# Optimization experiments

Measured on AMD Instinct MI355X. Metric: run time of the kernel, lower is better.

## Reference

```python
import jax, jax.numpy as jnp
from jax import lax
import numpy as np
import math

B, N, M, SIG, HID, NFEAT, OUT, H = 256, 512, 16, 256, 256, 3, 10, 256
ALPHA, BETA = 1.0, 0.5


def setup_inputs() -> dict:
    key = jax.random.key(0)
    ks = jax.random.split(key, 12)
    s_g = 1.0 / math.sqrt(HID)
    s_f = 1.0 / math.sqrt(SIG)
    return {
        "x": jax.random.normal(ks[0], (B, 1, H, H), jnp.float32),
        "unif": jax.random.uniform(ks[1], (B, N), jnp.float32),
        "z": jax.random.normal(ks[2], (B, N, 2), jnp.float32),
        "m_g_params": jax.random.normal(ks[3], (1, 6 * M), jnp.float32),
        "gc1_w": jax.random.uniform(ks[4], (NFEAT, HID), jnp.float32, -s_g, s_g),
        "gc1_b": jax.random.uniform(ks[5], (HID,), jnp.float32, -s_g, s_g),
        "gc2_w": jax.random.uniform(ks[6], (HID, HID), jnp.float32, -s_g, s_g),
        "gc2_b": jax.random.uniform(ks[7], (HID,), jnp.float32, -s_g, s_g),
        "collapser1": 0.1 * jax.random.normal(ks[8], (SIG, N), jnp.float32),
        "collapser2": 0.1 * jax.random.normal(ks[9], (SIG, N), jnp.float32),
        "fcf_w": jax.random.uniform(ks[10], (OUT, SIG), jnp.float32, -s_f, s_f),
        "fcf_b": jax.random.uniform(ks[11], (OUT,), jnp.float32, -s_f, s_f),
    }


def _mixture_fields(m_g_params):
    # torch: split [num_sample, 6M] into M chunks of 6, stack -> [M, N, 6],
    # split along last dim, then .view(N, M) in C-order on the [M, N] field.
    raw = m_g_params.reshape(M, 6)  # [M, 6]
    return [jnp.broadcast_to(raw[:, j][:, None], (M, N)).reshape(N, M) for j in range(6)]


def reference(x, unif, z, m_g_params, gc1_w, gc1_b, gc2_w, gc2_b,
              collapser1, collapser2, fcf_w, fcf_b):
    pi_f, mux_f, muy_f, sx_f, sy_f, rho_f = _mixture_fields(m_g_params)
    pi = jax.nn.softmax(pi_f, axis=-1)            # [N, M]
    # categorical sampling via CDF inversion, vectorized over batch
    cdf = jnp.cumsum(pi, axis=-1)                 # [N, M]
    idx = jnp.argmax(unif[:, :, None] < cdf[None], axis=-1)  # [B, N]
    row = jnp.arange(N)[None, :]
    gat = lambda f: f[row, idx]                   # [B, N]
    mux, muy = gat(mux_f), gat(muy_f)
    sx, sy = jnp.exp(gat(sx_f)), jnp.exp(gat(sy_f))
    rho = jnp.tanh(gat(rho_f))
    # reparameterized bivariate-normal sample via Cholesky (lower)
    z1, z2 = z[..., 0], z[..., 1]
    xs = mux + sx * z1
    ys = muy + sy * (rho * z1 + jnp.sqrt(1.0 - rho * rho) * z2)
    # torch MVN.sample() is no_grad -> detach samples
    xs_c, ys_c = lax.stop_gradient(xs), lax.stop_gradient(ys)
    dx, dy = xs_c - mux, ys_c - muy
    omr2 = 1.0 - rho * rho
    quad = (dx * dx / (sx * sx) - 2.0 * rho * dx * dy / (sx * sy) + dy * dy / (sy * sy)) / omr2
    logprob = (-jnp.log(2.0 * jnp.pi) - jnp.log(sx * sy)
               - 0.5 * jnp.log(omr2) - 0.5 * quad)  # [B, N]
    full_log_prob = logprob.sum(axis=-1)           # [B]
    loc = jnp.tanh(jnp.stack([xs_c, ys_c], axis=-1))  # [B, N, 2]
    # adjacency: inverse shifted pairwise squared distance
    diff = loc[:, :, None, :] - loc[:, None, :, :]  # [B, N, N, 2]
    adj = 1.0 / (ALPHA + BETA * jnp.sum(diff * diff, axis=-1))  # [B, N, N]
    # pixel gather: denormalize (trunc toward zero, like torch .long())
    pix = jnp.trunc(0.5 * (loc + 1.0) * H - 0.1).astype(jnp.int32)
    pix = jnp.clip(pix, 0, H - 1)
    bidx = jnp.arange(B)[:, None]
    pv = x[bidx, :, pix[..., 0], pix[..., 1]]      # [B, N, 1]
    feat = jnp.concatenate([pv, loc], axis=-1)     # [B, N, 3]
    # GCN (eval mode: no dropout)
    s1 = jax.nn.relu(jnp.einsum('bnm,bmh->bnh', adj, feat @ gc1_w) + gc1_b)
    s2 = jax.nn.relu(jnp.einsum('bnm,bmh->bnh', adj, s1 @ gc2_w) + gc2_b)
    # nn.Softmax() (no dim) on 3D input resolves to dim=0 in torch
    g1 = jax.nn.softmax(jnp.einsum('sn,bnh->bsh', collapser1, s1), axis=0)
    g2 = jax.nn.softmax(jnp.einsum('sn,bnh->bsh', collapser2, s2), axis=0)
    sig = (g1 + g2).sum(axis=2)                    # [B, SIG]
    out = jax.nn.softmax(sig @ fcf_w.T + fcf_b, axis=-1)  # [B, OUT]
    return out, full_log_prob
```

## Files before the change

kernel.cpp:

```cpp
#include <hip/hip_runtime.h>
#include <hip/hip_bf16.h>
#include <math.h>

#define Bx   256
#define Nx   512
#define SIGx 256
#define HIDx 256
#define OUTx 10
#define Hx   256

typedef __attribute__((ext_vector_type(4))) float f32x4;
typedef __attribute__((ext_vector_type(2))) uint uint2v;
typedef long fp8x8;
typedef unsigned char uchar;

#define WAITVM(N) asm volatile("s_waitcnt vmcnt(" #N ")" ::: "memory")
#define MEMFENCE() asm volatile("" ::: "memory")

__device__ inline uchar f2fp8(float v) {
    int r = __builtin_amdgcn_cvt_pk_fp8_f32(v, 0.0f, 0, false);
    return (uchar)(r & 0xff);
}
__device__ inline uint pk4fp8(float a0, float a1, float a2, float a3) {
    int r = __builtin_amdgcn_cvt_pk_fp8_f32(a0, a1, 0, false);
    r = __builtin_amdgcn_cvt_pk_fp8_f32(a2, a3, r, true);
    return (uint)r;
}

__device__ inline void gload_lds16(const uchar* g, uchar* l) {
    __builtin_amdgcn_global_load_lds(
        (const __attribute__((address_space(1))) uint*)g,
        (__attribute__((address_space(3))) uint*)l, 16, 0, 0);
}
__device__ inline const uchar* laddr(const uchar* base, int row, int kb) {
    int ps = (kb >> 4) ^ ((row >> 1) & 3) ^ ((row >> 4) & 3);
    return base + row*64 + ps*16 + (kb & 15);
}
__device__ inline const uchar* laddrB(const uchar* base, int row, int kb) {
    int ps = ((kb >> 4) & 7) ^ (row & 7);
    return base + row*128 + ps*16 + (kb & 15);
}

__global__ __launch_bounds__(512) void kA_sample(
    const float* __restrict__ x, const float* __restrict__ z,
    const float* __restrict__ mg, float* __restrict__ feat,
    float* __restrict__ flp)
{
    int b = blockIdx.x;
    int n = threadIdx.x;
    int g = n >> 5;
    float mux = mg[g*6+1];
    float muy = mg[g*6+2];
    float sxv = expf(mg[g*6+3]);
    float syv = expf(mg[g*6+4]);
    float rho = tanhf(mg[g*6+5]);
    float z1 = z[((size_t)b*Nx + n)*2 + 0];
    float z2 = z[((size_t)b*Nx + n)*2 + 1];
    float omr2 = 1.0f - rho*rho;
    float xs = mux + sxv*z1;
    float ys = muy + syv*(rho*z1 + sqrtf(omr2)*z2);
    float dx = xs - mux, dy = ys - muy;
    float quad = (dx*dx/(sxv*sxv) - 2.0f*rho*dx*dy/(sxv*syv) + dy*dy/(syv*syv)) / omr2;
    float logprob = -1.8378770664093453f - logf(sxv*syv) - 0.5f*logf(omr2) - 0.5f*quad;
    float lx = tanhf(xs), ly = tanhf(ys);
    int px = (int)truncf(0.5f*(lx+1.0f)*(float)Hx - 0.1f);
    int py = (int)truncf(0.5f*(ly+1.0f)*(float)Hx - 0.1f);
    px = px < 0 ? 0 : (px > Hx-1 ? Hx-1 : px);
    py = py < 0 ? 0 : (py > Hx-1 ? Hx-1 : py);
    float pv = x[(size_t)b*Hx*Hx + (size_t)px*Hx + py];
    size_t fo = ((size_t)b*Nx + n)*3;
    feat[fo+0] = pv; feat[fo+1] = lx; feat[fo+2] = ly;

    __shared__ float red[512];
    red[n] = logprob;
    __syncthreads();
    for (int st = 256; st > 0; st >>= 1) {
        if (n < st) red[n] += red[n+st];
        __syncthreads();
    }
    if (n == 0) flp[b] = red[0];
}

__global__ __launch_bounds__(256) void kPrep(
    const float* __restrict__ c1, const float* __restrict__ c2,
    const float* __restrict__ w2,
    uchar* __restrict__ c1q, uchar* __restrict__ c2q, uchar* __restrict__ w2tq)
{
    int idx = blockIdx.x*256 + threadIdx.x;
    if (idx < SIGx*Nx) {
        c1q[idx] = f2fp8(16.0f * c1[idx]);
        c2q[idx] = f2fp8(16.0f * c2[idx]);
    }
    if (idx < HIDx*HIDx) {
        int i = idx >> 8, j = idx & 255;
        w2tq[idx] = f2fp8(16.0f * w2[j*HIDx + i]);
    }
}

__global__ __launch_bounds__(512) void kFuse1S(
    const float* __restrict__ featL, const float* __restrict__ w1,
    const float* __restrict__ b1,
    uchar* __restrict__ adjAll, uchar* __restrict__ s1tAll)
{
    int b = blockIdx.x;
    int n0 = blockIdx.y * 256;
    const float* fb = featL + (size_t)b*Nx*3;
    uchar* adj = adjAll + (size_t)b*Nx*Nx;
    uchar* s1t = s1tAll + (size_t)b*HIDx*Nx;

    __shared__ float fpv[Nx], flx[Nx], fly[Nx], fH[Nx];
    __shared__ float w1s[3*HIDx], b1s[HIDx];
    __shared__ float Gp[8][3][256];

    int t = threadIdx.x;
    {
        float pv = fb[t*3+0], lx = fb[t*3+1], ly = fb[t*3+2];
        fpv[t] = pv; flx[t] = lx; fly[t] = ly;
        fH[t] = fmaf(0.5f*lx, lx, fmaf(0.5f*ly, ly, 1.0f));
    }
    for (int i = t; i < 3*HIDx; i += 512) w1s[i] = w1[i];
    if (t < HIDx) b1s[t] = b1[t];
    __syncthreads();

    int tq = t & 63;
    int mc = t >> 6;
    int lc = tq*4;
    int n4 = n0 + lc;

    float xn[4], yn[4], cn[4];
    #pragma unroll
    for (int e = 0; e < 4; ++e) {
        xn[e] = flx[n4+e]; yn[e] = fly[n4+e];
        cn[e] = fmaf(0.5f*xn[e], xn[e], 0.5f*yn[e]*yn[e]);
    }
    float G0[4] = {}, G1[4] = {}, G2[4] = {};

    int m0 = mc*64;
    #pragma unroll 4
    for (int mm = 0; mm < 64; ++mm) {
        int m = m0 + mm;
        float hx = fH[m], fx = flx[m], fy = fly[m];
        float a[4];
        #pragma unroll
        for (int e = 0; e < 4; ++e) {
            float s = fmaf(-yn[e], fy, fmaf(-xn[e], fx, hx + cn[e]));
            a[e] = __builtin_amdgcn_rcpf(s);
            G0[e] = fmaf(a[e], fpv[m], G0[e]);
            G1[e] = fmaf(a[e], fx, G1[e]);
            G2[e] = fmaf(a[e], fy, G2[e]);
        }
        *(uint*)(adj + (size_t)m*Nx + n4) = pk4fp8(a[0], a[1], a[2], a[3]);
    }

    *(f32x4*)&Gp[mc][0][lc] = (f32x4){G0[0],G0[1],G0[2],G0[3]};
    *(f32x4*)&Gp[mc][1][lc] = (f32x4){G1[0],G1[1],G1[2],G1[3]};
    *(f32x4*)&Gp[mc][2][lc] = (f32x4){G2[0],G2[1],G2[2],G2[3]};
    __syncthreads();

    f32x4 T0 = {}, T1 = {}, T2 = {};
    #pragma unroll
    for (int j = 0; j < 8; ++j) {
        T0 += *(const f32x4*)&Gp[j][0][lc];
        T1 += *(const f32x4*)&Gp[j][1][lc];
        T2 += *(const f32x4*)&Gp[j][2][lc];
    }

    int hc = mc;
    #pragma unroll 4
    for (int hh = 0; hh < 32; ++hh) {
        int h = hc*32 + hh;
        float w0 = w1s[h], wA = w1s[HIDx+h], wB = w1s[2*HIDx+h], bb = b1s[h];
        float v0 = fminf(fmaxf(fmaf(T0.x,w0, fmaf(T1.x,wA, fmaf(T2.x,wB, bb))), 0.0f), 448.0f);
        float v1 = fminf(fmaxf(fmaf(T0.y,w0, fmaf(T1.y,wA, fmaf(T2.y,wB, bb))), 0.0f), 448.0f);
        float v2 = fminf(fmaxf(fmaf(T0.z,w0, fmaf(T1.z,wA, fmaf(T2.z,wB, bb))), 0.0f), 448.0f);
        float v3 = fminf(fmaxf(fmaf(T0.w,w0, fmaf(T1.w,wA, fmaf(T2.w,wB, bb))), 0.0f), 448.0f);
        *(uint*)(s1t + (size_t)h*Nx + n4) = pk4fp8(v0, v1, v2, v3);
    }
}

__global__ __launch_bounds__(512, 4) void kGemmAdjB(
    const uchar* __restrict__ Aall, const uchar* __restrict__ adjAll,
    const float* __restrict__ bias, uchar* __restrict__ outAll)
{
    int b    = blockIdx.x;
    int tile = blockIdx.y;
    int rt = tile >> 2;
    int ct = tile & 3;
    const uchar* A = Aall + (size_t)b*HIDx*Nx;
    const uchar* Badj = adjAll + (size_t)b*Nx*Nx;
    uchar* outp = outAll + (size_t)b*HIDx*Nx;

    __shared__ __align__(16) uchar Als[2][128*128];
    __shared__ __align__(16) uchar Bls[2][128*128];
    int t = threadIdx.x;
    int lane = t & 63, wave = t >> 6;
    int wr = wave >> 2, wc = wave & 3;
    int q = lane >> 4, c16 = lane & 15;
    int r0 = rt*128, n0 = ct*128;
    int srow0 = t >> 3;
    int su0   = t & 7;
    f32x4 acc[4][2] = {};

    auto stage = [&](int buf, int kkv) {
        #pragma unroll
        for (int p = 0; p < 2; ++p) {
            int row = p*64 + srow0;
            int su = su0 ^ (row & 7);
            gload_lds16(A + (size_t)(r0+row)*Nx + kkv + su*16,
                        Als[buf] + p*8192 + wave*1024);
            gload_lds16(Badj + (size_t)(n0+row)*Nx + kkv + su*16,
                        Bls[buf] + p*8192 + wave*1024);
        }
    };

    const int nt = Nx/128;
    stage(0, 0);
    for (int i = 0; i < nt; ++i) {
        if (i < nt-1) { stage((i+1)&1, (i+1)*128); WAITVM(4); }
        else WAITVM(0);
        __builtin_amdgcn_s_barrier();
        MEMFENCE();
        const uchar* Ac = Als[i&1];
        const uchar* Bc = Bls[i&1];
        #pragma unroll
        for (int ks = 0; ks < 128; ks += 32) {
            fp8x8 af[4], bfr[2];
            #pragma unroll
            for (int i2 = 0; i2 < 4; ++i2)
                af[i2] = *(const fp8x8*)laddrB(Ac, wr*64 + i2*16 + c16, ks + q*8);
            #pragma unroll
            for (int j = 0; j < 2; ++j)
                bfr[j] = *(const fp8x8*)laddrB(Bc, wc*32 + j*16 + c16, ks + q*8);
            #pragma unroll
            for (int i2 = 0; i2 < 4; ++i2)
                #pragma unroll
                for (int j = 0; j < 2; ++j)
                    acc[i2][j] = __builtin_amdgcn_mfma_f32_16x16x32_fp8_fp8(af[i2], bfr[j], acc[i2][j], 0, 0, 0);
        }
        MEMFENCE();
        __builtin_amdgcn_s_barrier();
        MEMFENCE();
    }
    #pragma unroll
    for (int i = 0; i < 4; ++i) {
        int rowb = r0 + wr*64 + i*16 + q*4;
        #pragma unroll
        for (int j = 0; j < 2; ++j) {
            int col = n0 + wc*32 + j*16 + c16;
            #pragma unroll
            for (int r = 0; r < 4; ++r) {
                float v = fmaxf(acc[i][j][r] + bias[rowb + r], 0.0f) * 0.25f;
                outp[(size_t)(rowb + r)*Nx + col] = f2fp8(fminf(v, 448.0f));
            }
        }
    }
}

__global__ __launch_bounds__(512, 4) void kGstd8B(
    const uchar* __restrict__ Ash, const uchar* __restrict__ Ball,
    uchar* __restrict__ outAll, float oscale)
{
    int b    = blockIdx.x;
    int tile = blockIdx.y;
    int rt = tile >> 1;
    int ct = tile & 1;
    const uchar* B = Ball + (size_t)b*HIDx*Nx;
    uchar* outp = outAll + (size_t)b*HIDx*256;

    __shared__ __align__(16) uchar Als[2][128*128];
    __shared__ __align__(16) uchar Bls[2][128*128];
    int t = threadIdx.x;
    int lane = t & 63, wave = t >> 6;
    int wr = wave >> 2, wc = wave & 3;
    int q = lane >> 4, c16 = lane & 15;
    int r0 = rt*128, n0 = ct*128;
    int srow0 = t >> 3;
    int su0   = t & 7;
    f32x4 acc[4][2] = {};

    auto stage = [&](int buf, int kkv) {
        #pragma unroll
        for (int p = 0; p < 2; ++p) {
            int row = p*64 + srow0;
            int su = su0 ^ (row & 7);
            gload_lds16(Ash + (size_t)(r0+row)*Nx + kkv + su*16,
                        Als[buf] + p*8192 + wave*1024);
            gload_lds16(B + (size_t)(n0+row)*Nx + kkv + su*16,
                        Bls[buf] + p*8192 + wave*1024);
        }
    };

    const int nt = Nx/128;
    stage(0, 0);
    for (int i = 0; i < nt; ++i) {
        if (i < nt-1) { stage((i+1)&1, (i+1)*128); WAITVM(4); }
        else WAITVM(0);
        __builtin_amdgcn_s_barrier();
        MEMFENCE();
        const uchar* Ac = Als[i&1];
        const uchar* Bc = Bls[i&1];
        #pragma unroll
        for (int ks = 0; ks < 128; ks += 32) {
            fp8x8 af[4], bfr[2];
            #pragma unroll
            for (int i2 = 0; i2 < 4; ++i2)
                af[i2] = *(const fp8x8*)laddrB(Ac, wr*64 + i2*16 + c16, ks + q*8);
            #pragma unroll
            for (int j = 0; j < 2; ++j)
                bfr[j] = *(const fp8x8*)laddrB(Bc, wc*32 + j*16 + c16, ks + q*8);
            #pragma unroll
            for (int i2 = 0; i2 < 4; ++i2)
                #pragma unroll
                for (int j = 0; j < 2; ++j)
                    acc[i2][j] = __builtin_amdgcn_mfma_f32_16x16x32_fp8_fp8(af[i2], bfr[j], acc[i2][j], 0, 0, 0);
        }
        MEMFENCE();
        __builtin_amdgcn_s_barrier();
        MEMFENCE();
    }
    #pragma unroll
    for (int i = 0; i < 4; ++i) {
        int rowb = r0 + wr*64 + i*16 + q*4;
        #pragma unroll
        for (int j = 0; j < 2; ++j) {
            int col = n0 + wc*32 + j*16 + c16;
            #pragma unroll
            for (int r = 0; r < 4; ++r) {
                float v = acc[i][j][r] * oscale;
                v = fminf(fmaxf(v, -448.0f), 448.0f);
                outp[(size_t)(rowb + r)*256 + col] = f2fp8(v);
            }
        }
    }
}

__global__ __launch_bounds__(512, 4) void kGstdT8(
    const uchar* __restrict__ Ash, const uchar* __restrict__ Ball,
    uchar* __restrict__ outAll, float oscale)
{
    const int K = 256, NC = 512;
    int b    = blockIdx.x;
    int tile = blockIdx.y;
    int rt = tile >> 2;
    int ct = tile & 3;
    const uchar* B = Ball + (size_t)b*HIDx*Nx;
    uchar* outp = outAll + (size_t)b*HIDx*NC;

    __shared__ __align__(16) uchar Als[2][128*64];
    __shared__ __align__(16) uchar Bls[2][128*64];
    int t = threadIdx.x;
    int lane = t & 63, wave = t >> 6;
    int wr = wave >> 2, wc = wave & 3;
    int q = lane >> 4, c16 = lane & 15;
    int r0 = rt*128, n0 = ct*128;
    int srow = wave*16 + (lane >> 2);
    int pu   = lane & 3;
    int sl   = pu ^ ((srow>>1)&3) ^ ((srow>>4)&3);
    int pi  = t & 31;
    int g   = t >> 5;
    int nc8 = g & 7;
    int ch  = g >> 3;
    f32x4 acc[4][2] = {};

    auto stageA = [&](int buf, int kkv) {
        gload_lds16(Ash + (size_t)(r0+srow)*K + kkv + sl*16, Als[buf] + wave*1024);
    };
    auto loadBT = [&](int kkv, uint2v& v0, uint2v& v1) {
        int hk = kkv + 2*pi;
        const uchar* g0 = B + (size_t)hk*NC + n0 + nc8*16 + ch*8;
        v0 = *(const uint2v*)g0;
        v1 = *(const uint2v*)(g0 + NC);
    };
    auto writeBT = [&](int buf, const uint2v& v0, const uint2v& v1) {
        const uchar* pa = (const uchar*)&v0;
        const uchar* qa = (const uchar*)&v1;
        int kb = 2*pi;
        int s  = kb >> 4;
        #pragma unroll
        for (int e = 0; e < 8; ++e) {
            int row = nc8*16 + ch*8 + e;
            int ps = s ^ ((row>>1)&3) ^ ((row>>4)&3);
            *(ushort*)(Bls[buf] + row*64 + ps*16 + (kb & 15)) =
                (ushort)pa[e] | ((ushort)qa[e] << 8);
        }
    };
    auto mfmaStep = [&](int buf) {
        const uchar* Ac = Als[buf];
        const uchar* Bc = Bls[buf];
        #pragma unroll
        for (int ks = 0; ks < 64; ks += 32) {
            fp8x8 af[4], bfr[2];
            #pragma unroll
            for (int i = 0; i < 4; ++i)
                af[i] = *(const fp8x8*)laddr(Ac, wr*64 + i*16 + c16, ks + q*8);
            #pragma unroll
            for (int j = 0; j < 2; ++j)
                bfr[j] = *(const fp8x8*)laddr(Bc, wc*32 + j*16 + c16, ks + q*8);
            #pragma unroll
            for (int i = 0; i < 4; ++i)
                #pragma unroll
                for (int j = 0; j < 2; ++j)
                    acc[i][j] = __builtin_amdgcn_mfma_f32_16x16x32_fp8_fp8(af[i], bfr[j], acc[i][j], 0, 0, 0);
        }
    };

    uint2v bv0, bv1;
    stageA(0, 0);
    loadBT(0, bv0, bv1); writeBT(0, bv0, bv1);
    __syncthreads();
    for (int kk = 0; kk < K; kk += 64) {
        int cur = (kk >> 6) & 1, nxt = cur ^ 1;
        bool more = (kk + 64) < K;
        if (more) {
            stageA(nxt, kk + 64);
            loadBT(kk + 64, bv0, bv1);
        }
        mfmaStep(cur);
        if (more) writeBT(nxt, bv0, bv1);
        __syncthreads();
    }
    #pragma unroll
    for (int i = 0; i < 4; ++i) {
        int rowb = r0 + wr*64 + i*16 + q*4;
        #pragma unroll
        for (int j = 0; j < 2; ++j) {
            int col = n0 + wc*32 + j*16 + c16;
            #pragma unroll
            for (int r = 0; r < 4; ++r) {
                float v = acc[i][j][r] * oscale;
                v = fminf(fmaxf(v, -448.0f), 448.0f);
                outp[(size_t)(rowb + r)*NC + col] = f2fp8(v);
            }
        }
    }
}

__global__ __launch_bounds__(512) void kF1q(
    const uchar* __restrict__ t1, const uchar* __restrict__ t2,
    float* __restrict__ m1, float* __restrict__ rd1,
    float* __restrict__ m2, float* __restrict__ rd2)
{
    int s = blockIdx.x;
    int t = threadIdx.x;
    int hq = t & 63;
    int bq = t >> 6;
    const size_t str = (size_t)SIGx*HIDx;
    size_t base = (size_t)(bq*32)*str + (size_t)s*HIDx + hq*4;

    float mv1[4], dv1[4], mv2[4], dv2[4];
    #pragma unroll
    for (int e = 0; e < 4; ++e) { mv1[e]=-3.0e38f; dv1[e]=0.0f; mv2[e]=-3.0e38f; dv2[e]=0.0f; }

    for (int i = 0; i < 32; ++i) {
        uint u1 = *(const uint*)(t1 + base + (size_t)i*str);
        uint u2 = *(const uint*)(t2 + base + (size_t)i*str);
        float v1[4], v2[4];
        v1[0] = __builtin_amdgcn_cvt_f32_fp8(u1, 0);
        v1[1] = __builtin_amdgcn_cvt_f32_fp8(u1, 1);
        v1[2] = __builtin_amdgcn_cvt_f32_fp8(u1, 2);
        v1[3] = __builtin_amdgcn_cvt_f32_fp8(u1, 3);
        v2[0] = __builtin_amdgcn_cvt_f32_fp8(u2, 0);
        v2[1] = __builtin_amdgcn_cvt_f32_fp8(u2, 1);
        v2[2] = __builtin_amdgcn_cvt_f32_fp8(u2, 2);
        v2[3] = __builtin_amdgcn_cvt_f32_fp8(u2, 3);
        #pragma unroll
        for (int e = 0; e < 4; ++e) {
            float mn;
            mn = fmaxf(mv1[e], v1[e]);
            dv1[e] = dv1[e]*__expf(mv1[e]-mn) + __expf(v1[e]-mn); mv1[e] = mn;
            mn = fmaxf(mv2[e], v2[e]);
            dv2[e] = dv2[e]*__expf(mv2[e]-mn) + __expf(v2[e]-mn); mv2[e] = mn;
        }
    }

    __shared__ float pm1[8][256], pd1[8][256], pm2[8][256], pd2[8][256];
    #pragma unroll
    for (int e = 0; e < 4; ++e) {
        pm1[bq][hq*4+e] = mv1[e]; pd1[bq][hq*4+e] = dv1[e];
        pm2[bq][hq*4+e] = mv2[e]; pd2[bq][hq*4+e] = dv2[e];
    }
    __syncthreads();

    if (t < 256) {
        int h = t;
        float m = -3.0e38f, d = 0.0f;
        #pragma unroll
        for (int j = 0; j < 8; ++j) {
            float mm = pm1[j][h], dd = pd1[j][h];
            float mn = fmaxf(m, mm);
            d = d*__expf(m-mn) + dd*__expf(mm-mn);
            m = mn;
        }
        size_t o = (size_t)s*HIDx + h;
        m1[o] = m; rd1[o] = 1.0f/d;
    } else {
        int h = t - 256;
        float m = -3.0e38f, d = 0.0f;
        #pragma unroll
        for (int j = 0; j < 8; ++j) {
            float mm = pm2[j][h], dd = pd2[j][h];
            float mn = fmaxf(m, mm);
            d = d*__expf(m-mn) + dd*__expf(mm-mn);
            m = mn;
        }
        size_t o = (size_t)s*HIDx + h;
        m2[o] = m; rd2[o] = 1.0f/d;
    }
}

__global__ __launch_bounds__(256) void kF2q(
    const uchar* __restrict__ t1, const uchar* __restrict__ t2,
    const float* __restrict__ m1, const float* __restrict__ rd1,
    const float* __restrict__ m2, const float* __restrict__ rd2,
    float* __restrict__ sig)
{
    int b = blockIdx.y;
    int sq = threadIdx.x >> 6;
    int s = blockIdx.x*4 + sq;
    int hq = threadIdx.x & 63;
    size_t sh = (size_t)s*HIDx + hq*4;
    size_t tb = ((size_t)b*SIGx + s)*HIDx + hq*4;
    uint u1 = *(const uint*)(t1 + tb);
    uint u2 = *(const uint*)(t2 + tb);
    f32x4 a1 = *(const f32x4*)&m1[sh];
    f32x4 r1 = *(const f32x4*)&rd1[sh];
    f32x4 a2 = *(const f32x4*)&m2[sh];
    f32x4 r2 = *(const f32x4*)&rd2[sh];
    float v = 0.0f;
    v += __expf(__builtin_amdgcn_cvt_f32_fp8(u1,0) - a1.x) * r1.x;
    v += __expf(__builtin_amdgcn_cvt_f32_fp8(u1,1) - a1.y) * r1.y;
    v += __expf(__builtin_amdgcn_cvt_f32_fp8(u1,2) - a1.z) * r1.z;
    v += __expf(__builtin_amdgcn_cvt_f32_fp8(u1,3) - a1.w) * r1.w;
    v += __expf(__builtin_amdgcn_cvt_f32_fp8(u2,0) - a2.x) * r2.x;
    v += __expf(__builtin_amdgcn_cvt_f32_fp8(u2,1) - a2.y) * r2.y;
    v += __expf(__builtin_amdgcn_cvt_f32_fp8(u2,2) - a2.z) * r2.z;
    v += __expf(__builtin_amdgcn_cvt_f32_fp8(u2,3) - a2.w) * r2.w;

    __shared__ float red[256];
    red[threadIdx.x] = v;
    __syncthreads();
    for (int st = 32; st > 0; st >>= 1) {
        if (hq < st) red[threadIdx.x] += red[threadIdx.x + st];
        __syncthreads();
    }
    if (hq == 0) sig[(size_t)b*SIGx + s] = red[sq*64];
}

__global__ __launch_bounds__(256) void kG_out(
    const float* __restrict__ sig, const float* __restrict__ fw,
    const float* __restrict__ fb, float* __restrict__ out)
{
    int b = blockIdx.x;
    int tid = threadIdx.x;
    __shared__ float red[OUTx][257];
    float sv = sig[(size_t)b*SIGx + tid];
    #pragma unroll
    for (int o = 0; o < OUTx; ++o)
        red[o][tid] = sv * fw[o*SIGx + tid];
    __syncthreads();
    for (int st = 128; st > 0; st >>= 1) {
        if (tid < st) {
            #pragma unroll
            for (int o = 0; o < OUTx; ++o)
                red[o][tid] += red[o][tid + st];
        }
        __syncthreads();
    }
    if (tid == 0) {
        float logits[OUTx];
        float mx = -3.0e38f;
        #pragma unroll
        for (int o = 0; o < OUTx; ++o) {
            logits[o] = red[o][0] + fb[o];
            mx = fmaxf(mx, logits[o]);
        }
        float dd = 0.0f; float e[OUTx];
        #pragma unroll
        for (int o = 0; o < OUTx; ++o) { e[o] = expf(logits[o]-mx); dd += e[o]; }
        float inv = 1.0f/dd;
        #pragma unroll
        for (int o = 0; o < OUTx; ++o) out[(size_t)b*OUTx + o] = e[o]*inv;
    }
}

static inline size_t alignup(size_t b) { return (b + 255) & ~(size_t)255; }

extern "C" void kernel_launch(void* const* d_in, const int* in_sizes, int n_in,
                              void* d_out, int out_size, void* d_ws, size_t ws_size,
                              hipStream_t stream)
{
    const float* x   = (const float*)d_in[0];
    const float* z   = (const float*)d_in[2];
    const float* mg  = (const float*)d_in[3];
    const float* w1  = (const float*)d_in[4];
    const float* b1  = (const float*)d_in[5];
    const float* w2  = (const float*)d_in[6];
    const float* b2  = (const float*)d_in[7];
    const float* c1  = (const float*)d_in[8];
    const float* c2  = (const float*)d_in[9];
    const float* fw  = (const float*)d_in[10];
    const float* fbv = (const float*)d_in[11];
    float* out = (float*)d_out;
    float* flp = out + (size_t)Bx*OUTx;
    (void)in_sizes; (void)n_in; (void)out_size;

    char* ws = (char*)d_ws;
    size_t off = 0;
    auto alloc = [&](size_t bytes) -> char* {
        char* p = ws + off; off += alignup(bytes); return p;
    };
    float*  feat = (float*)alloc((size_t)Bx*Nx*3*4);
    uchar*  c1q  = (uchar*)alloc((size_t)SIGx*Nx);
    uchar*  c2q  = (uchar*)alloc((size_t)SIGx*Nx);
    uchar*  w2tq = (uchar*)alloc((size_t)HIDx*HIDx);
    uchar*  t1   = (uchar*)alloc((size_t)Bx*SIGx*HIDx);
    uchar*  t2   = (uchar*)alloc((size_t)Bx*SIGx*HIDx);
    float*  m1   = (float*)alloc((size_t)SIGx*HIDx*4);
    float*  d1   = (float*)alloc((size_t)SIGx*HIDx*4);
    float*  m2   = (float*)alloc((size_t)SIGx*HIDx*4);
    float*  d2   = (float*)alloc((size_t)SIGx*HIDx*4);
    float*  sig  = (float*)alloc((size_t)Bx*SIGx*4);
    size_t fixed = off;

    int BC = 1;
    for (int c = Bx; c >= 1; c >>= 1) {
        size_t need = fixed + alignup((size_t)c*Nx*Nx)
                            + 2*alignup((size_t)c*HIDx*Nx);
        if (need <= ws_size) { BC = c; break; }
    }
    uchar* Padj = (uchar*)alloc((size_t)BC*Nx*Nx);
    uchar* P1   = (uchar*)alloc((size_t)BC*HIDx*Nx);
    uchar* P2   = (uchar*)alloc((size_t)BC*HIDx*Nx);

    hipLaunchKernelGGL(kA_sample, dim3(Bx), dim3(Nx), 0, stream, x, z, mg, feat, flp);
    hipLaunchKernelGGL(kPrep, dim3(512), dim3(256), 0, stream, c1, c2, w2, c1q, c2q, w2tq);

    const int nch = Bx / BC;
    for (int c = 0; c < nch; ++c) {
        int b0 = c * BC;
        const float* featL = feat + (size_t)b0*Nx*3;
        uchar* t1L = t1 + (size_t)b0*SIGx*HIDx;
        uchar* t2L = t2 + (size_t)b0*SIGx*HIDx;
        hipLaunchKernelGGL(kFuse1S, dim3(BC, 2), dim3(512), 0, stream,
                           featL, w1, b1, Padj, P2);
        hipLaunchKernelGGL(kGstd8B, dim3(BC, 4), dim3(512), 0, stream,
                           c1q, P2, t1L, 0.0625f);
        hipLaunchKernelGGL(kGstdT8, dim3(BC, 8), dim3(512), 0, stream,
                           w2tq, P2, P1, 0.0625f);
        hipLaunchKernelGGL(kGemmAdjB, dim3(BC, 8), dim3(512), 0, stream, P1, Padj, b2, P2);
        hipLaunchKernelGGL(kGstd8B, dim3(BC, 4), dim3(512), 0, stream,
                           c2q, P2, t2L, 0.25f);
    }

    hipLaunchKernelGGL(kF1q, dim3(SIGx), dim3(512), 0, stream,
                       t1, t2, m1, d1, m2, d2);
    hipLaunchKernelGGL(kF2q, dim3(SIGx/4, Bx), dim3(256), 0, stream,
                       t1, t2, m1, d1, m2, d2, sig);
    hipLaunchKernelGGL(kG_out, dim3(Bx), dim3(256), 0, stream, sig, fw, fbv, out);
}
```

Before: 285.2 us.

## Remap GEMM blocks per XCD and shrink kGstd8 K-tile to 64

Flattens the 2D grids of the three per-batch GEMM kernels to 1D. A new xcd_chunk mapping puts all tiles of one batch element on the same XCD, so shared operands (adjacency, P1/P2) get reused in that XCD's L2 instead of being spread round-robin across chiplets. kGstd8 also moves to a 64-byte K step with the laddr swizzle, halving its LDS footprint, which may allow more resident blocks. The cost is twice as many K iterations and barriers in kGstd8.

```diff
diff --git a/kernel.cpp b/kernel.cpp
--- a/kernel.cpp
+++ b/kernel.cpp
@@ -39,6 +39,9 @@
 __device__ inline const uchar* laddrB(const uchar* base, int row, int kb) {
     int ps = ((kb >> 4) & 7) ^ (row & 7);
     return base + row*128 + ps*16 + (kb & 15);
+}
+__device__ inline int xcd_chunk(int bid, int nwg) {
+    return ((nwg & 7) == 0) ? ((bid & 7) * (nwg >> 3) + (bid >> 3)) : bid;
 }
 
 __global__ __launch_bounds__(512) void kA_sample(
@@ -182,8 +185,9 @@
     const uchar* __restrict__ Aall, const uchar* __restrict__ adjAll,
     const float* __restrict__ bias, uchar* __restrict__ outAll)
 {
-    int b    = blockIdx.x;
-    int tile = blockIdx.y;
+    int w = xcd_chunk(blockIdx.x, gridDim.x);
+    int b    = w >> 3;
+    int tile = w & 7;
     int rt = tile >> 2;
     int ct = tile & 3;
     const uchar* A = Aall + (size_t)b*HIDx*Nx;
@@ -256,58 +260,53 @@
     }
 }
 
-__global__ __launch_bounds__(512, 4) void kGstd8B(
+__global__ __launch_bounds__(512, 4) void kGstd8(
     const uchar* __restrict__ Ash, const uchar* __restrict__ Ball,
     uchar* __restrict__ outAll, float oscale)
 {
-    int b    = blockIdx.x;
-    int tile = blockIdx.y;
+    int w = xcd_chunk(blockIdx.x, gridDim.x);
+    int b    = w >> 2;
+    int tile = w & 3;
     int rt = tile >> 1;
     int ct = tile & 1;
     const uchar* B = Ball + (size_t)b*HIDx*Nx;
     uchar* outp = outAll + (size_t)b*HIDx*256;
 
-    __shared__ __align__(16) uchar Als[2][128*128];
-    __shared__ __align__(16) uchar Bls[2][128*128];
+    __shared__ __align__(16) uchar Als[2][128*64];
+    __shared__ __align__(16) uchar Bls[2][128*64];
     int t = threadIdx.x;
     int lane = t & 63, wave = t >> 6;
     int wr = wave >> 2, wc = wave & 3;
     int q = lane >> 4, c16 = lane & 15;
     int r0 = rt*128, n0 = ct*128;
-    int srow0 = t >> 3;
-    int su0   = t & 7;
+    int srow = wave*16 + (lane >> 2);
+    int pu   = lane & 3;
+    int sl   = pu ^ ((srow>>1)&3) ^ ((srow>>4)&3);
     f32x4 acc[4][2] = {};
 
     auto stage = [&](int buf, int kkv) {
-        #pragma unroll
-        for (int p = 0; p < 2; ++p) {
-            int row = p*64 + srow0;
-            int su = su0 ^ (row & 7);
-            gload_lds16(Ash + (size_t)(r0+row)*Nx + kkv + su*16,
-                        Als[buf] + p*8192 + wave*1024);
-            gload_lds16(B + (size_t)(n0+row)*Nx + kkv + su*16,
-                        Bls[buf] + p*8192 + wave*1024);
-        }
+        gload_lds16(Ash + (size_t)(r0+srow)*Nx + kkv + sl*16, Als[buf] + wave*1024);
+        gload_lds16(B + (size_t)(n0+srow)*Nx + kkv + sl*16, Bls[buf] + wave*1024);
     };
 
-    const int nt = Nx/128;
+    const int nt = Nx/64;
     stage(0, 0);
     for (int i = 0; i < nt; ++i) {
-        if (i < nt-1) { stage((i+1)&1, (i+1)*128); WAITVM(4); }
+        if (i < nt-1) { stage((i+1)&1, (i+1)*64); WAITVM(2); }
         else WAITVM(0);
         __builtin_amdgcn_s_barrier();
         MEMFENCE();
         const uchar* Ac = Als[i&1];
         const uchar* Bc = Bls[i&1];
         #pragma unroll
-        for (int ks = 0; ks < 128; ks += 32) {
+        for (int ks = 0; ks < 64; ks += 32) {
             fp8x8 af[4], bfr[2];
             #pragma unroll
             for (int i2 = 0; i2 < 4; ++i2)
-                af[i2] = *(const fp8x8*)laddrB(Ac, wr*64 + i2*16 + c16, ks + q*8);
+                af[i2] = *(const fp8x8*)laddr(Ac, wr*64 + i2*16 + c16, ks + q*8);
             #pragma unroll
             for (int j = 0; j < 2; ++j)
-                bfr[j] = *(const fp8x8*)laddrB(Bc, wc*32 + j*16 + c16, ks + q*8);
+                bfr[j] = *(const fp8x8*)laddr(Bc, wc*32 + j*16 + c16, ks + q*8);
             #pragma unroll
             for (int i2 = 0; i2 < 4; ++i2)
                 #pragma unroll
@@ -339,8 +338,9 @@
     uchar* __restrict__ outAll, float oscale)
 {
     const int K = 256, NC = 512;
-    int b    = blockIdx.x;
-    int tile = blockIdx.y;
+    int w = xcd_chunk(blockIdx.x, gridDim.x);
+    int b    = w >> 3;
+    int tile = w & 7;
     int rt = tile >> 2;
     int ct = tile & 3;
     const uchar* B = Ball + (size_t)b*HIDx*Nx;
@@ -643,12 +643,13 @@
         uchar* t2L = t2 + (size_t)b0*SIGx*HIDx;
         hipLaunchKernelGGL(kFuse1S, dim3(BC, 2), dim3(512), 0, stream,
                            featL, w1, b1, Padj, P2);
-        hipLaunchKernelGGL(kGstd8B, dim3(BC, 4), dim3(512), 0, stream,
+        hipLaunchKernelGGL(kGstd8, dim3(BC*4), dim3(512), 0, stream,
                            c1q, P2, t1L, 0.0625f);
-        hipLaunchKernelGGL(kGstdT8, dim3(BC, 8), dim3(512), 0, stream,
+        hipLaunchKernelGGL(kGstdT8, dim3(BC*8), dim3(512), 0, stream,
                            w2tq, P2, P1, 0.0625f);
-        hipLaunchKernelGGL(kGemmAdjB, dim3(BC, 8), dim3(512), 0, stream, P1, Padj, b2, P2);
-        hipLaunchKernelGGL(kGstd8B, dim3(BC, 4), dim3(512), 0, stream,
+        hipLaunchKernelGGL(kGemmAdjB, dim3(BC*8), dim3(512), 0, stream,
+                           P1, Padj, b2, P2);
+        hipLaunchKernelGGL(kGstd8, dim3(BC*4), dim3(512), 0, stream,
                            c2q, P2, t2L, 0.25f);
     }
 
```

New measurement: 279.7 us. About the same (-1.9%).
